# Performance work log

Hardware: AMD Instinct MI355X
Metric: run time of the kernel (lower is better)

Reference implementation:

```python
import jax, jax.numpy as jnp
import numpy as np

N = 100000   # nodes
E = 220000   # directed edges (each branch)
H = 128      # hidden_dim
OUT = 1      # output_dim
G = 4096     # num graphs in batch
PE = 5       # laplacian eigenvector PE dims
VOCAB = 28   # atom types


def gcn_conv(x, src, dst, W, b, n):
    # PyG GCNConv: x' = D^-1/2 (A + I) D^-1/2 (X W) + b
    h = x @ W
    deg = jax.ops.segment_sum(jnp.ones(src.shape[0], x.dtype), dst, num_segments=n) + 1.0
    dinv = jax.lax.rsqrt(deg)
    coef = dinv[src] * dinv[dst]                                    # [E]
    agg = jax.ops.segment_sum(h[src] * coef[:, None], dst, num_segments=n)
    agg = agg + h * (dinv * dinv)[:, None]                          # self-loop term
    return agg + b


def gcn2(x, edge_index, W1, b1, W2, b2, n):
    # PyG GCN model, num_layers=2: conv -> relu -> conv
    src, dst = edge_index[0], edge_index[1]
    h = jax.nn.relu(gcn_conv(x, src, dst, W1, b1, n))
    return gcn_conv(h, src, dst, W2, b2, n)


def setup_inputs() -> dict:
    key = jax.random.key(0)
    ks = jax.random.split(key, 16)
    s = 0.1
    return {
        "node_tokens": jax.random.randint(ks[0], (N, 1), 0, VOCAB),
        "pe": jax.random.normal(ks[1], (N, PE), jnp.float32),
        "edge_index": jax.random.randint(ks[2], (2, E), 0, N),
        "vr_edge_index": jax.random.randint(ks[3], (2, E), 0, N),
        "batch": jnp.sort(jax.random.randint(ks[4], (N,), 0, G)),
        "embed_table": jax.random.normal(ks[5], (VOCAB, H), jnp.float32) * s,
        "Wt": jax.random.normal(ks[6], (PE, H), jnp.float32) * s,
        "bt": jnp.zeros((H,), jnp.float32),
        "W1": jax.random.normal(ks[7], (H, H), jnp.float32) * s,
        "b1": jnp.zeros((H,), jnp.float32),
        "W2": jax.random.normal(ks[8], (H, OUT), jnp.float32) * s,
        "b2": jnp.zeros((OUT,), jnp.float32),
        "Wv1": jax.random.normal(ks[9], (H, H), jnp.float32) * s,
        "bv1": jnp.zeros((H,), jnp.float32),
        "Wv2": jax.random.normal(ks[10], (H, OUT), jnp.float32) * s,
        "bv2": jnp.zeros((OUT,), jnp.float32),
    }


def reference(node_tokens, pe, edge_index, vr_edge_index, batch, embed_table,
              Wt, bt, W1, b1, W2, b2, Wv1, bv1, Wv2, bv2):
    # embed_x(data.x.long()).squeeze(1) + lin_trans(pe)
    x = embed_table[node_tokens[:, 0]] + (pe @ Wt + bt)             # [N, H]
    x1 = gcn2(x, edge_index, W1, b1, W2, b2, N)                     # [N, OUT]
    xv = gcn2(x, vr_edge_index, Wv1, bv1, Wv2, bv2, N)              # [N, OUT]
    x1 = x1 + xv
    y_hat = jax.ops.segment_sum(x1, batch, num_segments=G)          # [G, OUT]
    y_hat = jnp.squeeze(y_hat, axis=-1)                             # [G]
    return (y_hat, x)
```

## Files before the change

kernel.cpp:

```cpp
#include <hip/hip_runtime.h>

#define NN 100000
#define NE 220000
#define HD 128
#define NG 4096
#define NPE 5
#define NB_SCAN ((NN + 255) / 256)
#define NBX4 ((NN * HD / 4) / 256)
#define NBG ((NN + 63) / 64)
#define NBW 128
#define NBZ ((2 * NN + 255) / 256)
#define NBE2 14
#define NBD ((2 * NE + 255) / 256)

typedef unsigned int uint;
typedef unsigned short ushort;
typedef __attribute__((ext_vector_type(8))) short bf16x8;
typedef __attribute__((ext_vector_type(4))) float f32x4;

__device__ __forceinline__ float bf2f(uint u16) {
    return __uint_as_float(u16 << 16);
}
__device__ __forceinline__ ushort f2bf(float f) {
    uint u = __float_as_uint(f);
    u += 0x7fffu + ((u >> 16) & 1u);
    return (ushort)(u >> 16);
}

__global__ void k_prep0(const float* __restrict__ W1, const float* __restrict__ Wv1,
                        const float* __restrict__ embed, const float* __restrict__ bt,
                        ushort* __restrict__ Wcat, int* __restrict__ cnt,
                        float* __restrict__ embed2) {
    int b = blockIdx.x;
    if (b < NBW) {
        int t = b * 256 + threadIdx.x;
        int f = t >> 7, k = t & 127;
        const float* W = (f < HD) ? W1 : Wv1;
        Wcat[t] = f2bf(W[k * HD + (f & 127)]);
    } else if (b < NBW + NBZ) {
        int t = (b - NBW) * 256 + threadIdx.x;
        if (t < 2 * NN) cnt[t] = 0;
    } else {
        int t = (b - NBW - NBZ) * 256 + threadIdx.x;
        if (t < 28 * 128) embed2[t] = embed[t] + bt[t & 127];
    }
}

__global__ void k_front(const int* __restrict__ tok, const float* __restrict__ pe,
                        const float* __restrict__ embed2, const float* __restrict__ Wtr,
                        float* __restrict__ x, ushort* __restrict__ xb,
                        const int* __restrict__ ei, const int* __restrict__ vei,
                        int* __restrict__ cnt) {
    int b = blockIdx.x;
    if (b < NBX4) {
        int idx = b * 256 + threadIdx.x;
        int n = idx >> 5, q = idx & 31;
        int t = tok[n];
        float4 acc = ((const float4*)(embed2 + (size_t)t * HD))[q];
        const float* pen = pe + n * NPE;
#pragma unroll
        for (int k = 0; k < NPE; ++k) {
            float p = pen[k];
            float4 wv = ((const float4*)(Wtr + k * HD))[q];
            acc.x += p * wv.x; acc.y += p * wv.y;
            acc.z += p * wv.z; acc.w += p * wv.w;
        }
        ((float4*)x)[idx] = acc;
        uint2 pk;
        pk.x = (uint)f2bf(acc.x) | ((uint)f2bf(acc.y) << 16);
        pk.y = (uint)f2bf(acc.z) | ((uint)f2bf(acc.w) << 16);
        ((uint2*)xb)[idx] = pk;
    } else {
        int t = (b - NBX4) * 256 + threadIdx.x;
        if (t < 2 * NE) {
            int br = t >= NE;
            int e = t - br * NE;
            const int* S = br ? vei : ei;
            atomicAdd(&cnt[br * NN + S[NE + e]], 1);
        }
    }
}

__global__ __launch_bounds__(256) void k_gemm(const ushort* __restrict__ xb,
                                              const ushort* __restrict__ Wt,
                                              ushort* __restrict__ H) {
    int bi = blockIdx.x;
    int fh = bi >= NBG;
    int b = bi - fh * NBG;
    int tid = threadIdx.x;
    int w = tid >> 6, lane = tid & 63;
    int m = lane & 15, quad = lane >> 4;
    int n = b * 64 + w * 16 + m;
    int nc = (n < NN) ? n : (NN - 1);
    const ushort* Arow = xb + (size_t)nc * HD + quad * 8;
    const ushort* Wg = Wt + (size_t)fh * 128 * 128 + (size_t)m * 128 + quad * 8;
    bf16x8 xf[4];
#pragma unroll
    for (int kc = 0; kc < 4; ++kc)
        xf[kc] = *(const bf16x8*)(Arow + kc * 32);
    f32x4 acc[8] = {};
#pragma unroll
    for (int ft = 0; ft < 8; ++ft) {
#pragma unroll
        for (int kc = 0; kc < 4; ++kc) {
            bf16x8 wf = *(const bf16x8*)(Wg + (size_t)ft * 16 * 128 + kc * 32);
            acc[ft] = __builtin_amdgcn_mfma_f32_16x16x32_bf16(wf, xf[kc], acc[ft], 0, 0, 0);
        }
    }
    if (n < NN) {
#pragma unroll
        for (int ft = 0; ft < 8; ++ft) {
            f32x4 a = acc[ft];
            uint2 pk;
            pk.x = (uint)f2bf(a[0]) | ((uint)f2bf(a[1]) << 16);
            pk.y = (uint)f2bf(a[2]) | ((uint)f2bf(a[3]) << 16);
            *(uint2*)&H[(size_t)n * 256 + fh * 128 + ft * 16 + quad * 4] = pk;
        }
    }
}

__global__ void k_scan1(const int* __restrict__ cnt, int* __restrict__ off,
                        int* __restrict__ bsum, float* __restrict__ dinv,
                        float* __restrict__ y) {
    __shared__ int s[256];
    int tid = threadIdx.x;
    int gid = blockIdx.x * 256 + tid;
    if (gid < NG) y[gid] = 0.f;
    int br = blockIdx.x / NB_SCAN;
    int blk = blockIdx.x % NB_SCAN;
    int i = blk * 256 + tid;
    int v = (i < NN) ? cnt[br * NN + i] : 0;
    if (i < NN) dinv[br * NN + i] = rsqrtf((float)v + 1.0f);
    s[tid] = v;
    __syncthreads();
    for (int d = 1; d < 256; d <<= 1) {
        int t = (tid >= d) ? s[tid - d] : 0;
        __syncthreads();
        s[tid] += t;
        __syncthreads();
    }
    if (i < NN) off[br * NN + i] = s[tid] - v;
    if (tid == 255) bsum[br * 512 + blk] = s[255];
}

__global__ void k_scan3(const int* __restrict__ off, const int* __restrict__ bsum,
                        const int* __restrict__ cnt, int2* __restrict__ off2,
                        int* __restrict__ cur) {
    __shared__ int s[256];
    int br = blockIdx.x / NB_SCAN;
    int blk = blockIdx.x % NB_SCAN;
    int tid = threadIdx.x;
    int v = 0;
    if (tid < blk) v = bsum[br * 512 + tid];
    if (tid + 256 < blk) v += bsum[br * 512 + tid + 256];
    s[tid] = v;
#pragma unroll
    for (int d = 128; d > 0; d >>= 1) {
        __syncthreads();
        if (tid < d) s[tid] += s[tid + d];
    }
    __syncthreads();
    int pre = s[0];
    int i = blk * 256 + tid;
    if (i < NN) {
        int o = off[br * NN + i] + pre;
        int2 pr;
        pr.x = o;
        pr.y = o + cnt[br * NN + i];
        off2[br * NN + i] = pr;
        cur[br * NN + i] = o;
    }
}

__global__ void k_scatter(const int* __restrict__ ei, const int* __restrict__ vei,
                          const float* __restrict__ dinv, int* __restrict__ cur,
                          int2* __restrict__ ent) {
    int t = blockIdx.x * blockDim.x + threadIdx.x;
    if (t >= 2 * NE) return;
    int br = t >= NE;
    int e = t - br * NE;
    const int* S = br ? vei : ei;
    int s = S[e], d = S[NE + e];
    int pos = atomicAdd(&cur[br * NN + d], 1);
    int2 rec;
    rec.x = s;
    rec.y = __float_as_int(dinv[br * NN + s] * dinv[br * NN + d]);
    ent[br * NE + pos] = rec;
}

__global__ void k_gather_ep(const ushort* __restrict__ H, const float* __restrict__ dinv,
                            const int2* __restrict__ off2,
                            const int2* __restrict__ ent,
                            const float* __restrict__ b1, const float* __restrict__ bv1,
                            const float* __restrict__ W2, const float* __restrict__ Wv2,
                            float* __restrict__ z) {
    int wid = threadIdx.x >> 6;
    int lane = threadIdx.x & 63;
    int half = lane >> 5;
    int l = lane & 31;
    int task = blockIdx.x * 8 + wid * 2 + half;
    int br = task >= NN;
    int n = task - br * NN;

    const int2* en = ent + br * NE;
    size_t hoff = (size_t)br * 128;

    float dv = dinv[br * NN + n];
    uint2 u = *(const uint2*)(H + (size_t)n * 256 + hoff + l * 4);
    float c = dv * dv;
    float a0 = bf2f(u.x & 0xffffu) * c, a1 = bf2f(u.x >> 16) * c;
    float a2 = bf2f(u.y & 0xffffu) * c, a3 = bf2f(u.y >> 16) * c;

    int2 pr = off2[br * NN + n];
    int p0 = pr.x, p1 = pr.y;
    for (int p = p0; p < p1; p += 4) {
        int2 e0 = en[p], e1 = en[p + 1], e2 = en[p + 2], e3 = en[p + 3];
        int s0 = e0.x;
        int s1 = (p + 1 < p1) ? e1.x : n;
        int s2 = (p + 2 < p1) ? e2.x : n;
        int s3 = (p + 3 < p1) ? e3.x : n;
        float c0 = __int_as_float(e0.y);
        float c1 = (p + 1 < p1) ? __int_as_float(e1.y) : 0.f;
        float c2 = (p + 2 < p1) ? __int_as_float(e2.y) : 0.f;
        float c3 = (p + 3 < p1) ? __int_as_float(e3.y) : 0.f;
        uint2 v0 = *(const uint2*)(H + (size_t)s0 * 256 + hoff + l * 4);
        uint2 v1 = *(const uint2*)(H + (size_t)s1 * 256 + hoff + l * 4);
        uint2 v2 = *(const uint2*)(H + (size_t)s2 * 256 + hoff + l * 4);
        uint2 v3 = *(const uint2*)(H + (size_t)s3 * 256 + hoff + l * 4);
        a0 += bf2f(v0.x & 0xffffu) * c0; a1 += bf2f(v0.x >> 16) * c0;
        a2 += bf2f(v0.y & 0xffffu) * c0; a3 += bf2f(v0.y >> 16) * c0;
        a0 += bf2f(v1.x & 0xffffu) * c1; a1 += bf2f(v1.x >> 16) * c1;
        a2 += bf2f(v1.y & 0xffffu) * c1; a3 += bf2f(v1.y >> 16) * c1;
        a0 += bf2f(v2.x & 0xffffu) * c2; a1 += bf2f(v2.x >> 16) * c2;
        a2 += bf2f(v2.y & 0xffffu) * c2; a3 += bf2f(v2.y >> 16) * c2;
        a0 += bf2f(v3.x & 0xffffu) * c3; a1 += bf2f(v3.x >> 16) * c3;
        a2 += bf2f(v3.y & 0xffffu) * c3; a3 += bf2f(v3.y >> 16) * c3;
    }

    const float* bb = br ? bv1 : b1;
    const float* ww = br ? Wv2 : W2;
    float4 b4 = *(const float4*)&bb[l * 4];
    float4 w4 = *(const float4*)&ww[l * 4];
    float part = fmaxf(a0 + b4.x, 0.f) * w4.x + fmaxf(a1 + b4.y, 0.f) * w4.y
               + fmaxf(a2 + b4.z, 0.f) * w4.z + fmaxf(a3 + b4.w, 0.f) * w4.w;
#pragma unroll
    for (int o = 16; o > 0; o >>= 1) part += __shfl_down(part, o, 32);
    if (l == 0) z[br * NN + n] = part;
}

__global__ void k_final2(const float* __restrict__ z, const float* __restrict__ dinv,
                         const int2* __restrict__ off2,
                         const int2* __restrict__ ent,
                         const float* __restrict__ b2, const float* __restrict__ bv2,
                         const int* __restrict__ batch, float* __restrict__ y) {
    __shared__ float ybuf[256];
    __shared__ int gbase_s;
    int br = blockIdx.x >= NB_SCAN;
    int nb = blockIdx.x - br * NB_SCAN;
    int tid = threadIdx.x;
    ybuf[tid] = 0.f;
    if (tid == 0) gbase_s = batch[nb * 256];
    __syncthreads();
    int gbase = gbase_s;
    int n = nb * 256 + tid;
    if (n < NN) {
        const int2* en = ent + br * NE;
        float dv = dinv[br * NN + n];
        float acc = z[br * NN + n] * dv * dv;
        int2 pr = off2[br * NN + n];
        int p1 = pr.y;
        for (int p = pr.x; p < p1; p += 4) {
            int2 e0 = en[p], e1 = en[p + 1], e2 = en[p + 2], e3 = en[p + 3];
            int s0 = e0.x;
            int s1 = (p + 1 < p1) ? e1.x : n;
            int s2 = (p + 2 < p1) ? e2.x : n;
            int s3 = (p + 3 < p1) ? e3.x : n;
            float c0 = __int_as_float(e0.y);
            float c1 = (p + 1 < p1) ? __int_as_float(e1.y) : 0.f;
            float c2 = (p + 2 < p1) ? __int_as_float(e2.y) : 0.f;
            float c3 = (p + 3 < p1) ? __int_as_float(e3.y) : 0.f;
            acc += c0 * z[br * NN + s0] + c1 * z[br * NN + s1]
                 + c2 * z[br * NN + s2] + c3 * z[br * NN + s3];
        }
        acc += br ? bv2[0] : b2[0];
        int gi = batch[n] - gbase;
        if (gi < 256) atomicAdd(&ybuf[gi], acc);
        else atomicAdd(&y[batch[n]], acc);
    }
    __syncthreads();
    float v = ybuf[tid];
    if (v != 0.f) atomicAdd(&y[gbase + tid], v);
}

extern "C" void kernel_launch(void* const* d_in, const int* in_sizes, int n_in,
                              void* d_out, int out_size, void* d_ws, size_t ws_size,
                              hipStream_t stream) {
    const int*   tok   = (const int*)d_in[0];
    const float* pe    = (const float*)d_in[1];
    const int*   ei    = (const int*)d_in[2];
    const int*   vei   = (const int*)d_in[3];
    const int*   batch = (const int*)d_in[4];
    const float* embed = (const float*)d_in[5];
    const float* Wtr   = (const float*)d_in[6];
    const float* bt    = (const float*)d_in[7];
    const float* W1    = (const float*)d_in[8];
    const float* b1    = (const float*)d_in[9];
    const float* W2    = (const float*)d_in[10];
    const float* b2    = (const float*)d_in[11];
    const float* Wv1   = (const float*)d_in[12];
    const float* bv1   = (const float*)d_in[13];
    const float* Wv2   = (const float*)d_in[14];
    const float* bv2   = (const float*)d_in[15];

    float* y = (float*)d_out;
    float* x = y + NG;

    char* w = (char*)d_ws;
    ushort* xb   = (ushort*)w;               w += (size_t)NN * HD * 2;
    ushort* H    = (ushort*)w;               w += (size_t)NN * 256 * 2;
    ushort* Wcat = (ushort*)w;               w += 256 * 128 * 2;
    float*  emb2 = (float*)w;                w += 28 * 128 * 4;
    float*  dinv = (float*)w;                w += 2 * NN * 4;
    float*  z    = (float*)w;                w += 2 * NN * 4;
    int*    cnt  = (int*)w;                  w += 2 * NN * 4;
    int*    off  = (int*)w;                  w += 2 * NN * 4;
    int*    cur  = (int*)w;                  w += 2 * NN * 4;
    int2*   off2 = (int2*)w;                 w += (size_t)2 * NN * 8;
    int2*   ent  = (int2*)w;                 w += (size_t)(2 * NE + 8) * 8;
    int*    bsum = (int*)w;                  w += 2 * 512 * 4;

    k_prep0<<<NBW + NBZ + NBE2, 256, 0, stream>>>(W1, Wv1, embed, bt, Wcat, cnt, emb2);
    k_front<<<NBX4 + NBD, 256, 0, stream>>>(tok, pe, emb2, Wtr, x, xb, ei, vei, cnt);
    k_gemm<<<2 * NBG, 256, 0, stream>>>(xb, Wcat, H);
    k_scan1<<<2 * NB_SCAN, 256, 0, stream>>>(cnt, off, bsum, dinv, y);
    k_scan3<<<2 * NB_SCAN, 256, 0, stream>>>(off, bsum, cnt, off2, cur);
    k_scatter<<<NBD, 256, 0, stream>>>(ei, vei, dinv, cur, ent);
    k_gather_ep<<<2 * NN / 8, 256, 0, stream>>>(H, dinv, off2, ent,
                                                b1, bv1, W2, Wv2, z);
    k_final2<<<2 * NB_SCAN, 256, 0, stream>>>(z, dinv, off2, ent,
                                              b2, bv2, batch, y);
}
```

Baseline: 262.1 us.

## Make GEMM persistent with weights held in registers across node tiles

The GEMM becomes a persistent kernel with 1024 blocks. Each wave loads its 64-column slice of the concatenated weight matrix into registers once, then grid-strides over 16-node tiles. Previously each block reloaded weight fragments for every 64-node tile and every half. This removes repeated weight loads, but each x row is now read by all four waves of a block, and register pressure rises from holding 16 bf16x8 fragments. The bounds check is dropped because NN divides evenly by 16.

```diff
diff --git a/kernel.cpp b/kernel.cpp
--- a/kernel.cpp
+++ b/kernel.cpp
@@ -7,7 +7,8 @@
 #define NPE 5
 #define NB_SCAN ((NN + 255) / 256)
 #define NBX4 ((NN * HD / 4) / 256)
-#define NBG ((NN + 63) / 64)
+#define NT16 (NN / 16)
+#define NBGEMM 1024
 #define NBW 128
 #define NBZ ((2 * NN + 255) / 256)
 #define NBE2 14
@@ -84,37 +85,38 @@
 __global__ __launch_bounds__(256) void k_gemm(const ushort* __restrict__ xb,
                                               const ushort* __restrict__ Wt,
                                               ushort* __restrict__ H) {
-    int bi = blockIdx.x;
-    int fh = bi >= NBG;
-    int b = bi - fh * NBG;
-    int tid = threadIdx.x;
-    int w = tid >> 6, lane = tid & 63;
+    int w = threadIdx.x >> 6;
+    int lane = threadIdx.x & 63;
     int m = lane & 15, quad = lane >> 4;
-    int n = b * 64 + w * 16 + m;
-    int nc = (n < NN) ? n : (NN - 1);
-    const ushort* Arow = xb + (size_t)nc * HD + quad * 8;
-    const ushort* Wg = Wt + (size_t)fh * 128 * 128 + (size_t)m * 128 + quad * 8;
-    bf16x8 xf[4];
-#pragma unroll
-    for (int kc = 0; kc < 4; ++kc)
-        xf[kc] = *(const bf16x8*)(Arow + kc * 32);
-    f32x4 acc[8] = {};
-#pragma unroll
-    for (int ft = 0; ft < 8; ++ft) {
-#pragma unroll
-        for (int kc = 0; kc < 4; ++kc) {
-            bf16x8 wf = *(const bf16x8*)(Wg + (size_t)ft * 16 * 128 + kc * 32);
-            acc[ft] = __builtin_amdgcn_mfma_f32_16x16x32_bf16(wf, xf[kc], acc[ft], 0, 0, 0);
-        }
-    }
-    if (n < NN) {
-#pragma unroll
-        for (int ft = 0; ft < 8; ++ft) {
-            f32x4 a = acc[ft];
+    const ushort* Wbase = Wt + ((size_t)(w * 4) * 16 + m) * 128 + quad * 8;
+    bf16x8 wf[4][4];
+#pragma unroll
+    for (int j = 0; j < 4; ++j)
+#pragma unroll
+        for (int kc = 0; kc < 4; ++kc)
+            wf[j][kc] = *(const bf16x8*)(Wbase + (size_t)j * 16 * 128 + kc * 32);
+
+    for (int t = blockIdx.x; t < NT16; t += NBGEMM) {
+        int n = t * 16 + m;
+        const ushort* Arow = xb + (size_t)n * HD + quad * 8;
+        bf16x8 xf[4];
+#pragma unroll
+        for (int kc = 0; kc < 4; ++kc)
+            xf[kc] = *(const bf16x8*)(Arow + kc * 32);
+        f32x4 acc[4] = {};
+#pragma unroll
+        for (int j = 0; j < 4; ++j)
+#pragma unroll
+            for (int kc = 0; kc < 4; ++kc)
+                acc[j] = __builtin_amdgcn_mfma_f32_16x16x32_bf16(wf[j][kc], xf[kc],
+                                                                 acc[j], 0, 0, 0);
+#pragma unroll
+        for (int j = 0; j < 4; ++j) {
+            f32x4 a = acc[j];
             uint2 pk;
             pk.x = (uint)f2bf(a[0]) | ((uint)f2bf(a[1]) << 16);
             pk.y = (uint)f2bf(a[2]) | ((uint)f2bf(a[3]) << 16);
-            *(uint2*)&H[(size_t)n * 256 + fh * 128 + ft * 16 + quad * 4] = pk;
+            *(uint2*)&H[(size_t)n * 256 + (w * 4 + j) * 16 + quad * 4] = pk;
         }
     }
 }
@@ -331,7 +333,7 @@
 
     k_prep0<<<NBW + NBZ + NBE2, 256, 0, stream>>>(W1, Wv1, embed, bt, Wcat, cnt, emb2);
     k_front<<<NBX4 + NBD, 256, 0, stream>>>(tok, pe, emb2, Wtr, x, xb, ei, vei, cnt);
-    k_gemm<<<2 * NBG, 256, 0, stream>>>(xb, Wcat, H);
+    k_gemm<<<NBGEMM, 256, 0, stream>>>(xb, Wcat, H);
     k_scan1<<<2 * NB_SCAN, 256, 0, stream>>>(cnt, off, bsum, dinv, y);
     k_scan3<<<2 * NB_SCAN, 256, 0, stream>>>(off, bsum, cnt, off2, cur);
     k_scatter<<<NBD, 256, 0, stream>>>(ei, vei, dinv, cur, ent);
```

New measurement: 231.7 us. -11.6%, faster.
